# Performance work log

Measured on AMD Instinct MI355X. Metric: run time of the kernel, lower is better.

## Reference

```python
import jax, jax.numpy as jnp
import numpy as np
import math

B, S, D, H = 2, 2048, 1024, 16
DK = D // H

def setup_inputs() -> dict:
    key = jax.random.key(0)
    ks = jax.random.split(key, 12)
    s = 1.0 / math.sqrt(D)
    inp = {
        'input_q': jax.random.normal(ks[0], (B, S, D), jnp.float32),
        'input_k': jax.random.normal(ks[1], (B, S, D), jnp.float32),
        'input_v': jax.random.normal(ks[2], (B, S, D), jnp.float32),
        'mask': jax.random.randint(ks[3], (B, 1, S, S), 0, 2, jnp.int32),
        'Wq': jax.random.normal(ks[4], (D, D), jnp.float32) * s,
        'bq': jnp.zeros((D,), jnp.float32),
        'Wk': jax.random.normal(ks[5], (D, D), jnp.float32) * s,
        'bk': jnp.zeros((D,), jnp.float32),
        'Wv': jax.random.normal(ks[6], (D, D), jnp.float32) * s,
        'bv': jnp.zeros((D,), jnp.float32),
        'Wo': jax.random.normal(ks[7], (D, D), jnp.float32) * s,
        'bo': jnp.zeros((D,), jnp.float32),
    }
    return inp

def reference(input_q, input_k, input_v, mask, Wq, bq, Wk, bk, Wv, bv, Wo, bo):
    # Linear projections (torch Linear: x @ W.T + b), split into heads: [B,H,S,DK]
    q = (input_q @ Wq.T + bq).reshape(B, S, H, DK).transpose(0, 2, 1, 3)
    k = (input_k @ Wk.T + bk).reshape(B, S, H, DK).transpose(0, 2, 1, 3)
    v = (input_v @ Wv.T + bv).reshape(B, S, H, DK).transpose(0, 2, 1, 3)
    scores = jnp.einsum('bhqd,bhkd->bhqk', q, k) / math.sqrt(DK)
    scores = jnp.where(mask == 0, jnp.float32(-1e9), scores)
    attn = jax.nn.softmax(scores, axis=-1)
    out = jnp.einsum('bhqk,bhkd->bhqd', attn, v)
    out = out.transpose(0, 2, 1, 3).reshape(B, S, D)
    return out @ Wo.T + bo
```

## Files before the change

### kernel.cpp

```cpp
#include <hip/hip_runtime.h>
#include <math.h>

#define kB 2
#define kS 2048
#define kD 1024
#define kH 16
#define kM (kB * kS)

#define kC 0.180336880f

typedef unsigned short u16;
typedef unsigned int u32;
typedef unsigned long long u64;
typedef short s16x8 __attribute__((ext_vector_type(8)));
typedef float f32x4 __attribute__((ext_vector_type(4)));

#if __has_builtin(__builtin_amdgcn_exp2f)
#define EXP2(x) __builtin_amdgcn_exp2f(x)
#else
#define EXP2(x) exp2f(x)
#endif

__device__ __forceinline__ u16 f2bf(float f) {
    u32 u = __float_as_uint(f);
    u += 0x7FFFu + ((u >> 16) & 1u);
    return (u16)(u >> 16);
}

__device__ __forceinline__ u32 cvt_pk_bf16(float lo, float hi) {
    u32 r;
    asm("v_cvt_pk_bf16_f32 %0, %1, %2" : "=v"(r) : "v"(lo), "v"(hi));
    return r;
}

typedef __attribute__((address_space(1))) void as1_void;
typedef __attribute__((address_space(3))) void as3_void;
__device__ __forceinline__ void async_copy16(const void* g, void* l) {
    __builtin_amdgcn_global_load_lds((as1_void*)(unsigned long long)g,
                                     (as3_void*)(unsigned)(unsigned long long)l,
                                     16, 0, 0);
}

__global__ __launch_bounds__(256) void prep(
        const float* __restrict__ xq, const float* __restrict__ xk, const float* __restrict__ xv,
        const float* __restrict__ Wq, const float* __restrict__ Wk,
        const float* __restrict__ Wv, const float* __restrict__ Wo,
        const int* __restrict__ msk,
        u16* __restrict__ xqb, u16* __restrict__ xkb, u16* __restrict__ xvb,
        u16* __restrict__ wqb, u16* __restrict__ wkb, u16* __restrict__ wvb,
        u16* __restrict__ wob, u64* __restrict__ prepM) {
    const int bid = blockIdx.x;
    const int tid = threadIdx.x;
    if (bid < 16384) {
        const float* in;
        u16* out;
        int i;
        float sc = 1.0f;
        if (bid < 12288) {
            const int z = bid >> 12;
            in = z == 0 ? xq : (z == 1 ? xk : xv);
            out = z == 0 ? xqb : (z == 1 ? xkb : xvb);
            i = (bid & 4095) * 256 + tid;
        } else {
            const int z = (bid - 12288) >> 10;
            in = z == 0 ? Wq : (z == 1 ? Wk : (z == 2 ? Wv : Wo));
            out = z == 0 ? wqb : (z == 1 ? wkb : (z == 2 ? wvb : wob));
            if (z == 0) sc = kC;
            i = ((bid - 12288) & 1023) * 256 + tid;
        }
        const float4 v = ((const float4*)in)[i];
        ushort4 o;
        o.x = f2bf(v.x * sc); o.y = f2bf(v.y * sc);
        o.z = f2bf(v.z * sc); o.w = f2bf(v.w * sc);
        ((ushort4*)out)[i] = o;
    } else {
        const int wid = (bid - 16384) * 4 + (tid >> 6);
        const int lane = tid & 63;
        const int kt = wid & 31, qb = (wid >> 5) & 127, b = wid >> 12;
        const int q = qb * 16 + (lane & 15);
        const int kbase = kt * 64 + ((lane >> 4) << 2);
        const int* mrow = msk + ((size_t)b * kS + q) * kS;
        u64 keep = 0;
#pragma unroll
        for (int c = 0; c < 4; ++c) {
            const int4 m4 = *(const int4*)(mrow + kbase + c * 16);
            const int mv[4] = {m4.x, m4.y, m4.z, m4.w};
#pragma unroll
            for (int r = 0; r < 4; ++r) {
                const u64 bl = __ballot(mv[r] != 0);
                if (lane == c * 4 + r) keep = bl;
            }
        }
        if (lane < 16)
            prepM[(((size_t)b * 128 + qb) * 32 + kt) * 16 + lane] = keep;
    }
}

template <int MODE, int TILEM>
__device__ __forceinline__ void gemm_bt_body(const u16* __restrict__ A,
                                             const u16* __restrict__ W,
                                             const float* __restrict__ bias,
                                             void* __restrict__ Cp,
                                             const float bscale,
                                             u16* __restrict__ AsM,
                                             u16* __restrict__ BsM) {
    constexpr int FM = TILEM / 32;
    u16* As0 = AsM;            u16* As1 = AsM + TILEM * 32;
    u16* Bs0 = BsM;            u16* Bs1 = BsM + 128 * 32;
    const int tid = threadIdx.x;
    const int wave = tid >> 6, lane = tid & 63;
    const int l15 = lane & 15, quad = lane >> 4;
    const int wr = wave >> 1, wc = wave & 1;
    const int m0 = (MODE == 3 ? blockIdx.x : blockIdx.y) * TILEM;
    const int n0 = (MODE == 3 ? blockIdx.y : blockIdx.x) * 128;

    const int srow = lane >> 2;
    const int schk = ((lane & 3) - ((lane >> 3) & 3)) & 3;
    const u16* gA = A + (size_t)(m0 + (TILEM / 4) * wave + srow) * kD + schk * 8;
    const u16* gB = W + (size_t)(n0 + 32 * wave + srow) * kD + schk * 8;

    f32x4 acc[FM][4];
#pragma unroll
    for (int i = 0; i < FM; ++i)
#pragma unroll
        for (int j = 0; j < 4; ++j) acc[i][j] = (f32x4)0.f;

    auto STAGE = [&](int kt, u16* dA, u16* dB) {
#pragma unroll
        for (int i = 0; i < TILEM / 64; ++i)
            async_copy16(gA + (size_t)(16 * i) * kD + kt,
                         dA + (wave * (TILEM / 64) + i) * 512);
#pragma unroll
        for (int i = 0; i < 2; ++i)
            async_copy16(gB + (size_t)(16 * i) * kD + kt,
                         dB + (wave * 2 + i) * 512);
    };

    const int ro = ((quad + (l15 >> 1)) & 3) * 8;
    auto COMPUTE = [&](const u16* sA, const u16* sB) {
        s16x8 af[FM], bf[4];
#pragma unroll
        for (int fm = 0; fm < FM; ++fm)
            af[fm] = *(const s16x8*)(sA + (wr * (TILEM / 32) + fm) * 512 + l15 * 32 + ro);
#pragma unroll
        for (int fn = 0; fn < 4; ++fn)
            bf[fn] = *(const s16x8*)(sB + (wc * 4 + fn) * 512 + l15 * 32 + ro);
#pragma unroll
        for (int fm = 0; fm < FM; ++fm)
#pragma unroll
            for (int fn = 0; fn < 4; ++fn)
                acc[fm][fn] = __builtin_amdgcn_mfma_f32_16x16x32_bf16(
                    af[fm], bf[fn], acc[fm][fn], 0, 0, 0);
    };

    STAGE(0, As0, Bs0);
    __syncthreads();
    for (int kt = 0; kt < kD; kt += 64) {
        if (kt + 32 < kD) STAGE(kt + 32, As1, Bs1);
        COMPUTE(As0, Bs0);
        __syncthreads();
        if (kt + 64 < kD) STAGE(kt + 64, As0, Bs0);
        COMPUTE(As1, Bs1);
        __syncthreads();
    }

    if constexpr (MODE == 3) {
#pragma unroll
        for (int fn = 0; fn < 4; ++fn) {
            const int sglob = n0 + wc * 64 + fn * 16 + l15;
            const int bb = sglob >> 11, ss = sglob & (kS - 1);
#pragma unroll
            for (int fm = 0; fm < FM; ++fm) {
                const int dglob = m0 + wr * (TILEM / 2) + fm * 16 + quad * 4;
                const float4 b4 = *(const float4*)(bias + dglob);
                const float bb4[4] = {b4.x * bscale, b4.y * bscale,
                                      b4.z * bscale, b4.w * bscale};
                const int hh = dglob >> 6, dd = dglob & 63;
                u16* base = (u16*)Cp + ((size_t)(bb * kH + hh) * 64 + dd) * kS + ss;
#pragma unroll
                for (int r = 0; r < 4; ++r)
                    base[(size_t)r * kS] = f2bf(acc[fm][fn][r] + bb4[r]);
            }
        }
    } else {
#pragma unroll
        for (int fn = 0; fn < 4; ++fn) {
            const int col = n0 + wc * 64 + fn * 16 + l15;
            const float bv = bias[col] * bscale;
#pragma unroll
            for (int fm = 0; fm < FM; ++fm) {
                const int row = m0 + wr * (TILEM / 2) + fm * 16 + quad * 4;
#pragma unroll
                for (int r = 0; r < 4; ++r) {
                    const float v = acc[fm][fn][r] + bv;
                    if constexpr (MODE == 0)
                        ((u16*)Cp)[(size_t)(row + r) * kD + col] = f2bf(v);
                    else
                        ((float*)Cp)[(size_t)(row + r) * kD + col] = v;
                }
            }
        }
    }
}

__global__ __launch_bounds__(256) void qkv_gemm(
        const u16* __restrict__ xq, const u16* __restrict__ xk, const u16* __restrict__ xv,
        const u16* __restrict__ wq, const u16* __restrict__ wk, const u16* __restrict__ wv,
        const float* __restrict__ bq, const float* __restrict__ bk, const float* __restrict__ bv,
        u16* __restrict__ q, u16* __restrict__ k, u16* __restrict__ vt) {
    __shared__ u16 AsM[2 * 128 * 32];
    __shared__ u16 BsM[2 * 128 * 32];
    const int z = blockIdx.z;
    if (z == 0)      gemm_bt_body<0, 128>(xq, wq, bq, q, kC, AsM, BsM);
    else if (z == 1) gemm_bt_body<0, 128>(xk, wk, bk, k, 1.f, AsM, BsM);
    else             gemm_bt_body<3, 128>(wv, xv, bv, vt, 1.f, AsM, BsM);
}

__global__ __launch_bounds__(256) void o_gemm(const u16* __restrict__ A,
                                              const u16* __restrict__ W,
                                              const float* __restrict__ bias,
                                              float* __restrict__ C) {
    __shared__ u16 AsM[2 * 64 * 32];
    __shared__ u16 BsM[2 * 128 * 32];
    gemm_bt_body<2, 64>(A, W, bias, C, 1.f, AsM, BsM);
}

__device__ __forceinline__ void attn_tile(
        const int kt, u16* __restrict__ cur, u16* __restrict__ nxt, const bool do_stage,
        const u16* __restrict__ gK0, const u16* __restrict__ gV0,
        const u64* __restrict__ mbase,
        const s16x8 bq0, const s16x8 bq1, const s16x8 onesf,
        u16* __restrict__ psrow,
        f32x4 oacc[4], f32x4& lacc,
        const int l15, const int quad, const int l7, const int wave) {
    if (do_stage) {
        async_copy16(gK0 + (size_t)(kt + 64) * kD, nxt + (8 * wave) * 64);
        async_copy16(gV0 + kt + 64, nxt + 4096 + (8 * wave) * 64);
    }
    const u64* mt = mbase + (kt >> 6) * 16;
    u64 mk[16];
#pragma unroll
    for (int i = 0; i < 16; ++i) mk[i] = mt[i];

    f32x4 s[4];
#pragma unroll
    for (int fn = 0; fn < 4; ++fn) s[fn] = (f32x4)0.f;
    __builtin_amdgcn_s_setprio(1);
#pragma unroll
    for (int kc = 0; kc < 2; ++kc) {
        const s16x8 bqf = kc ? bq1 : bq0;
#pragma unroll
        for (int fn = 0; fn < 4; ++fn) {
            const s16x8 ak = *(const s16x8*)(cur + (fn * 16 + l15) * 64 + ((kc * 4 + quad) ^ l7) * 8);
            s[fn] = __builtin_amdgcn_mfma_f32_16x16x32_bf16(ak, bqf, s[fn], 0, 0, 0);
        }
    }
    __builtin_amdgcn_s_setprio(0);

    s16x8 av[2][4];
#pragma unroll
    for (int kc = 0; kc < 2; ++kc)
#pragma unroll
        for (int fd = 0; fd < 4; ++fd)
            av[kc][fd] = *(const s16x8*)(cur + 4096 + (fd * 16 + l15) * 64 + ((kc * 4 + quad) ^ l7) * 8);

#pragma unroll
    for (int fn = 0; fn < 4; ++fn)
#pragma unroll
        for (int r = 0; r < 4; ++r) {
            const float p = EXP2(s[fn][r]);
            float pm;
            asm("v_cndmask_b32 %0, 0, %1, %2" : "=v"(pm) : "v"(p), "s"(mk[fn * 4 + r]));
            s[fn][r] = pm;
        }

#pragma unroll
    for (int fn = 0; fn < 4; ++fn) {
        uint2 o;
        o.x = cvt_pk_bf16(s[fn][0], s[fn][1]);
        o.y = cvt_pk_bf16(s[fn][2], s[fn][3]);
        const int chunk = fn * 2 + (quad >> 1);
        *(uint2*)(psrow + ((chunk ^ l7) * 8) + (quad & 1) * 4) = o;
    }

    __builtin_amdgcn_s_setprio(1);
#pragma unroll
    for (int kc = 0; kc < 2; ++kc) {
        const s16x8 bp = *(const s16x8*)(psrow + ((kc * 4 + quad) ^ l7) * 8);
        lacc = __builtin_amdgcn_mfma_f32_16x16x32_bf16(onesf, bp, lacc, 0, 0, 0);
#pragma unroll
        for (int fd = 0; fd < 4; ++fd)
            oacc[fd] = __builtin_amdgcn_mfma_f32_16x16x32_bf16(av[kc][fd], bp, oacc[fd], 0, 0, 0);
    }
    __builtin_amdgcn_s_setprio(0);
    __syncthreads();
}

__global__ __launch_bounds__(512) void attn_mfma(const u16* __restrict__ Qb,
                                                 const u16* __restrict__ Kb,
                                                 const u16* __restrict__ Vt,
                                                 const u64* __restrict__ prepM,
                                                 u16* __restrict__ Ob) {
    __shared__ u16 Bs2[2][8192];
    __shared__ u16 Ps[8192];

    const int tid = threadIdx.x;
    const int wave = tid >> 6, lane = tid & 63;
    const int l15 = lane & 15, quad = lane >> 4, l7 = lane & 7;
    const int q0 = blockIdx.x * 128;
    const int b = blockIdx.y >> 4, h = blockIdx.y & 15;

    const int srow = lane >> 3;
    const int schk = l7 ^ srow;

    {
        const u16* g0 = Qb + ((size_t)(b * kS + q0 + 16 * wave + srow)) * kD + h * 64 + schk * 8;
        async_copy16(g0, Ps + (16 * wave) * 64);
        async_copy16(g0 + 8 * kD, Ps + (16 * wave + 8) * 64);
    }
    const u16* gK0 = Kb + ((size_t)(b * kS + 8 * wave + srow)) * kD + h * 64 + schk * 8;
    const u16* gV0 = Vt + ((size_t)((b * kH + h) * 64 + 8 * wave + srow)) * kS + schk * 8;
    async_copy16(gK0, Bs2[0] + (8 * wave) * 64);
    async_copy16(gV0, Bs2[0] + 4096 + (8 * wave) * 64);

    const int wave_u = __builtin_amdgcn_readfirstlane(wave);
    const u64* mbase = prepM + (((size_t)b * 128 + blockIdx.x * 8 + wave_u) * 32) * 16;

    s16x8 onesf;
#pragma unroll
    for (int i = 0; i < 8; ++i) onesf[i] = (short)0x3F80;

    f32x4 oacc[4];
#pragma unroll
    for (int i = 0; i < 4; ++i) oacc[i] = (f32x4)0.f;
    f32x4 lacc = (f32x4)0.f;

    __syncthreads();
    s16x8 bq0, bq1;
    bq0 = *(const s16x8*)(Ps + (16 * wave + l15) * 64 + ((0 + quad) ^ l7) * 8);
    bq1 = *(const s16x8*)(Ps + (16 * wave + l15) * 64 + ((4 + quad) ^ l7) * 8);
    u16* psrow = Ps + (16 * wave + l15) * 64;

    for (int ti = 0; ti < 32; ti += 2) {
        attn_tile(ti * 64, Bs2[0], Bs2[1], true,
                  gK0, gV0, mbase, bq0, bq1, onesf, psrow, oacc, lacc,
                  l15, quad, l7, wave);
        attn_tile(ti * 64 + 64, Bs2[1], Bs2[0], ti + 2 < 32,
                  gK0, gV0, mbase, bq0, bq1, onesf, psrow, oacc, lacc,
                  l15, quad, l7, wave);
    }

    const float inv = 1.f / lacc[0];
    const size_t orow = (size_t)(b * kS + q0 + 16 * wave + l15);
#pragma unroll
    for (int fd = 0; fd < 4; ++fd) {
        uint2 o;
        o.x = cvt_pk_bf16(oacc[fd][0] * inv, oacc[fd][1] * inv);
        o.y = cvt_pk_bf16(oacc[fd][2] * inv, oacc[fd][3] * inv);
        *(uint2*)(Ob + orow * kD + h * 64 + fd * 16 + quad * 4) = o;
    }
}

extern "C" void kernel_launch(void* const* d_in, const int* in_sizes, int n_in,
                              void* d_out, int out_size, void* d_ws, size_t ws_size,
                              hipStream_t stream) {
    const float* xq = (const float*)d_in[0];
    const float* xk = (const float*)d_in[1];
    const float* xv = (const float*)d_in[2];
    const int*  msk = (const int*)d_in[3];
    const float* Wq = (const float*)d_in[4];
    const float* bq = (const float*)d_in[5];
    const float* Wk = (const float*)d_in[6];
    const float* bk = (const float*)d_in[7];
    const float* Wv = (const float*)d_in[8];
    const float* bv = (const float*)d_in[9];
    const float* Wo = (const float*)d_in[10];
    const float* bo = (const float*)d_in[11];
    float* out = (float*)d_out;

    const size_t NX = (size_t)kM * kD;
    const size_t NW = (size_t)kD * kD;

    u64* prepM = (u64*)d_ws;
    u16* p = (u16*)((char*)d_ws + (1 << 20));
    u16* xqb = p; p += NX;
    u16* xkb = p; p += NX;
    u16* xvb = p; p += NX;
    u16* wqb = p; p += NW;
    u16* wkb = p; p += NW;
    u16* wvb = p; p += NW;
    u16* wob = p; p += NW;
    u16* qb  = p; p += NX;
    u16* kb  = p; p += NX;
    u16* vtb = p; p += NX;
    u16* ab  = xqb;

    prep<<<18432, 256, 0, stream>>>(xq, xk, xv, Wq, Wk, Wv, Wo, msk,
                                    xqb, xkb, xvb, wqb, wkb, wvb, wob, prepM);

    dim3 gq(kD / 128, kM / 128, 3);
    qkv_gemm<<<gq, 256, 0, stream>>>(xqb, xkb, xvb, wqb, wkb, wvb, bq, bk, bv, qb, kb, vtb);

    dim3 ga(kS / 128, kB * kH);
    attn_mfma<<<ga, 512, 0, stream>>>(qb, kb, vtb, prepM, ab);

    dim3 go(kD / 128, kM / 64);
    o_gemm<<<go, 256, 0, stream>>>(ab, wob, bo, out);
}
```

Measured before the change: 254.5 us.

## Halve GEMM N-tile to 64 and remap block IDs for XCD locality

The GEMM body now takes a TILEN template parameter, and the QKV and output projections switch from a 128-wide to a 64-wide N tile, which doubles the number of blocks per launch. Block indices are no longer taken straight from blockIdx. They are remapped from a linear id, grouped by id & 7, so that blocks landing on the same XCD share input or weight tiles in cache. The aim is more parallelism to fill the CUs and better L2 reuse. The cost is lower arithmetic intensity per block and more repeated loads of A tiles.

Measured after the change: 244.8 us. 3.8% less time.

```diff
diff --git a/kernel.cpp b/kernel.cpp
--- a/kernel.cpp
+++ b/kernel.cpp
@@ -96,34 +96,36 @@
     }
 }
 
-template <int MODE, int TILEM>
+template <int MODE, int TILEM, int TILEN>
 __device__ __forceinline__ void gemm_bt_body(const u16* __restrict__ A,
                                              const u16* __restrict__ W,
                                              const float* __restrict__ bias,
                                              void* __restrict__ Cp,
                                              const float bscale,
                                              u16* __restrict__ AsM,
-                                             u16* __restrict__ BsM) {
+                                             u16* __restrict__ BsM,
+                                             const int bxi, const int byi) {
     constexpr int FM = TILEM / 32;
+    constexpr int FN = TILEN / 32;
     u16* As0 = AsM;            u16* As1 = AsM + TILEM * 32;
-    u16* Bs0 = BsM;            u16* Bs1 = BsM + 128 * 32;
+    u16* Bs0 = BsM;            u16* Bs1 = BsM + TILEN * 32;
     const int tid = threadIdx.x;
     const int wave = tid >> 6, lane = tid & 63;
     const int l15 = lane & 15, quad = lane >> 4;
     const int wr = wave >> 1, wc = wave & 1;
-    const int m0 = (MODE == 3 ? blockIdx.x : blockIdx.y) * TILEM;
-    const int n0 = (MODE == 3 ? blockIdx.y : blockIdx.x) * 128;
+    const int m0 = (MODE == 3 ? bxi : byi) * TILEM;
+    const int n0 = (MODE == 3 ? byi : bxi) * TILEN;
 
     const int srow = lane >> 2;
     const int schk = ((lane & 3) - ((lane >> 3) & 3)) & 3;
     const u16* gA = A + (size_t)(m0 + (TILEM / 4) * wave + srow) * kD + schk * 8;
-    const u16* gB = W + (size_t)(n0 + 32 * wave + srow) * kD + schk * 8;
-
-    f32x4 acc[FM][4];
+    const u16* gB = W + (size_t)(n0 + (TILEN / 4) * wave + srow) * kD + schk * 8;
+
+    f32x4 acc[FM][FN];
 #pragma unroll
     for (int i = 0; i < FM; ++i)
 #pragma unroll
-        for (int j = 0; j < 4; ++j) acc[i][j] = (f32x4)0.f;
+        for (int j = 0; j < FN; ++j) acc[i][j] = (f32x4)0.f;
 
     auto STAGE = [&](int kt, u16* dA, u16* dB) {
 #pragma unroll
@@ -131,24 +133,24 @@
             async_copy16(gA + (size_t)(16 * i) * kD + kt,
                          dA + (wave * (TILEM / 64) + i) * 512);
 #pragma unroll
-        for (int i = 0; i < 2; ++i)
+        for (int i = 0; i < TILEN / 64; ++i)
             async_copy16(gB + (size_t)(16 * i) * kD + kt,
-                         dB + (wave * 2 + i) * 512);
+                         dB + (wave * (TILEN / 64) + i) * 512);
     };
 
     const int ro = ((quad + (l15 >> 1)) & 3) * 8;
     auto COMPUTE = [&](const u16* sA, const u16* sB) {
-        s16x8 af[FM], bf[4];
+        s16x8 af[FM], bf[FN];
 #pragma unroll
         for (int fm = 0; fm < FM; ++fm)
             af[fm] = *(const s16x8*)(sA + (wr * (TILEM / 32) + fm) * 512 + l15 * 32 + ro);
 #pragma unroll
-        for (int fn = 0; fn < 4; ++fn)
-            bf[fn] = *(const s16x8*)(sB + (wc * 4 + fn) * 512 + l15 * 32 + ro);
+        for (int fn = 0; fn < FN; ++fn)
+            bf[fn] = *(const s16x8*)(sB + (wc * (TILEN / 32) + fn) * 512 + l15 * 32 + ro);
 #pragma unroll
         for (int fm = 0; fm < FM; ++fm)
 #pragma unroll
-            for (int fn = 0; fn < 4; ++fn)
+            for (int fn = 0; fn < FN; ++fn)
                 acc[fm][fn] = __builtin_amdgcn_mfma_f32_16x16x32_bf16(
                     af[fm], bf[fn], acc[fm][fn], 0, 0, 0);
     };
@@ -166,8 +168,8 @@
 
     if constexpr (MODE == 3) {
 #pragma unroll
-        for (int fn = 0; fn < 4; ++fn) {
-            const int sglob = n0 + wc * 64 + fn * 16 + l15;
+        for (int fn = 0; fn < FN; ++fn) {
+            const int sglob = n0 + wc * (TILEN / 2) + fn * 16 + l15;
             const int bb = sglob >> 11, ss = sglob & (kS - 1);
 #pragma unroll
             for (int fm = 0; fm < FM; ++fm) {
@@ -184,8 +186,8 @@
         }
     } else {
 #pragma unroll
-        for (int fn = 0; fn < 4; ++fn) {
-            const int col = n0 + wc * 64 + fn * 16 + l15;
+        for (int fn = 0; fn < FN; ++fn) {
+            const int col = n0 + wc * (TILEN / 2) + fn * 16 + l15;
             const float bv = bias[col] * bscale;
 #pragma unroll
             for (int fm = 0; fm < FM; ++fm) {
@@ -209,11 +211,20 @@
         const float* __restrict__ bq, const float* __restrict__ bk, const float* __restrict__ bv,
         u16* __restrict__ q, u16* __restrict__ k, u16* __restrict__ vt) {
     __shared__ u16 AsM[2 * 128 * 32];
-    __shared__ u16 BsM[2 * 128 * 32];
+    __shared__ u16 BsM[2 * 64 * 32];
+    const int id = blockIdx.y * 16 + blockIdx.x;
+    const int g = id & 7, mm = id >> 3;
     const int z = blockIdx.z;
-    if (z == 0)      gemm_bt_body<0, 128>(xq, wq, bq, q, kC, AsM, BsM);
-    else if (z == 1) gemm_bt_body<0, 128>(xk, wk, bk, k, 1.f, AsM, BsM);
-    else             gemm_bt_body<3, 128>(wv, xv, bv, vt, 1.f, AsM, BsM);
+    if (z == 2) {
+        const int bm = mm >> 3;
+        const int bn = g * 8 + (mm & 7);
+        gemm_bt_body<3, 128, 64>(wv, xv, bv, vt, 1.f, AsM, BsM, bm, bn);
+    } else {
+        const int by = g * 4 + (mm & 3);
+        const int bx = mm >> 2;
+        if (z == 0) gemm_bt_body<0, 128, 64>(xq, wq, bq, q, kC, AsM, BsM, bx, by);
+        else        gemm_bt_body<0, 128, 64>(xk, wk, bk, k, 1.f, AsM, BsM, bx, by);
+    }
 }
 
 __global__ __launch_bounds__(256) void o_gemm(const u16* __restrict__ A,
@@ -221,8 +232,12 @@
                                               const float* __restrict__ bias,
                                               float* __restrict__ C) {
     __shared__ u16 AsM[2 * 64 * 32];
-    __shared__ u16 BsM[2 * 128 * 32];
-    gemm_bt_body<2, 64>(A, W, bias, C, 1.f, AsM, BsM);
+    __shared__ u16 BsM[2 * 64 * 32];
+    const int id = blockIdx.y * 16 + blockIdx.x;
+    const int g = id & 7, mm = id >> 3;
+    const int by = g * 8 + (mm & 7);
+    const int bx = mm >> 3;
+    gemm_bt_body<2, 64, 64>(A, W, bias, C, 1.f, AsM, BsM, bx, by);
 }
 
 __device__ __forceinline__ void attn_tile(
@@ -398,12 +413,12 @@
     prep<<<18432, 256, 0, stream>>>(xq, xk, xv, Wq, Wk, Wv, Wo, msk,
                                     xqb, xkb, xvb, wqb, wkb, wvb, wob, prepM);
 
-    dim3 gq(kD / 128, kM / 128, 3);
+    dim3 gq(kD / 64, kM / 128, 3);
     qkv_gemm<<<gq, 256, 0, stream>>>(xqb, xkb, xvb, wqb, wkb, wvb, bq, bk, bv, qb, kb, vtb);
 
     dim3 ga(kS / 128, kB * kH);
     attn_mfma<<<ga, 512, 0, stream>>>(qb, kb, vtb, prepM, ab);
 
-    dim3 go(kD / 128, kM / 64);
+    dim3 go(kD / 64, kM / 64);
     o_gemm<<<go, 256, 0, stream>>>(ab, wob, bo, out);
 }
```
